# Performance work log

Measured on AMD Instinct MI355X. Metric: run time of the kernel, lower is better.

## Reference

```python
import jax, jax.numpy as jnp
import numpy as np

N_NODES = 20000
N_EDGES = 320000
IN_F = 256
OUT_F = 64
HEADS = 4
ALPHA = 0.1  # leaky_relu negative slope


def setup_inputs() -> dict:
    key = jax.random.key(0)
    ks = jax.random.split(key, 8)
    return {
        "input1": jax.random.normal(ks[0], (N_NODES, IN_F), jnp.float32),
        "input2": jax.random.normal(ks[1], (N_NODES, IN_F), jnp.float32),
        # per-head params: Ws maps source feats -> target_out, Wt maps target feats -> source_out
        "Ws": jax.random.normal(ks[2], (HEADS, IN_F, OUT_F), jnp.float32) * 0.06,
        "Wt": jax.random.normal(ks[3], (HEADS, IN_F, OUT_F), jnp.float32) * 0.06,
        "a1": jax.random.normal(ks[4], (HEADS, 2 * OUT_F), jnp.float32) * 0.1,
        "a2": jax.random.normal(ks[5], (HEADS, 2 * OUT_F), jnp.float32) * 0.1,
        # COO nonzeros of A_opt [n_target, n_source]
        "tgt_idx": jax.random.randint(ks[6], (N_EDGES,), 0, N_NODES),
        "src_idx": jax.random.randint(ks[7], (N_EDGES,), 0, N_NODES),
    }


def _segment_softmax(scores, seg, num_segments):
    m = jax.lax.stop_gradient(jax.ops.segment_max(scores, seg, num_segments=num_segments))
    w = jnp.exp(scores - m[seg])
    d = jax.ops.segment_sum(w, seg, num_segments=num_segments)
    d = jnp.where(d == 0, 1.0, d)
    return w / d[seg]


def _head(x1, x2, Ws, Wt, a1, a2, src, tgt, n_s, n_t):
    s = x1 @ Ws  # [n_s, OUT_F]  messages source -> target
    t = x2 @ Wt  # [n_t, OUT_F]  messages target -> source
    out = Ws.shape[1]
    # edge score e = leaky_relu(a^T [s_src || t_tgt]); split a to avoid edge-level concat
    e1 = jax.nn.leaky_relu((s @ a1[:out])[src] + (t @ a1[out:])[tgt], ALPHA)
    e2 = jax.nn.leaky_relu((s @ a2[:out])[src] + (t @ a2[out:])[tgt], ALPHA)
    alpha_ts = _segment_softmax(e1, tgt, n_t)  # softmax over sources per target
    alpha_st = _segment_softmax(e2, src, n_s)  # softmax over targets per source
    h_ts = jax.ops.segment_sum(alpha_ts[:, None] * s[src], tgt, num_segments=n_t)
    h_st = jax.ops.segment_sum(alpha_st[:, None] * t[tgt], src, num_segments=n_s)
    return jax.nn.elu(h_st), jax.nn.elu(h_ts)  # concat=True -> ELU per head


def reference(input1, input2, Ws, Wt, a1, a2, tgt_idx, src_idx):
    n_s, n_t = input1.shape[0], input2.shape[0]
    head_fn = jax.vmap(
        lambda W1, W2, v1, v2: _head(input1, input2, W1, W2, v1, v2, src_idx, tgt_idx, n_s, n_t)
    )
    h_st, h_ts = head_fn(Ws, Wt, a1, a2)  # each [H, n, OUT_F]
    h_st = jnp.transpose(h_st, (1, 0, 2)).reshape(n_s, -1)  # concat heads
    h_ts = jnp.transpose(h_ts, (1, 0, 2)).reshape(n_t, -1)
    return h_st, h_ts
```

## Files before the change

kernel.cpp:

```cpp
#include <hip/hip_runtime.h>
#include <math.h>

#define N_NODES 20000
#define N_EDGES 320000
#define IN_F 256
#define OUT_F 64
#define HEADS 4
#define NCOL 256
#define LRELU_ALPHA 0.1f
#define ELL_CAP 64

#define SCAT_X 313
#define GEMM_GB 157
#define CST_STRIDE 136

typedef __attribute__((ext_vector_type(8))) short short8;
typedef __attribute__((ext_vector_type(4))) float floatx4;

__device__ __forceinline__ float lrelu(float x) {
    return x > 0.f ? x : LRELU_ALPHA * x;
}
__device__ __forceinline__ unsigned short f2bf(float f) {
    unsigned int u = __float_as_uint(f);
    u = (u + 0x7FFF + ((u >> 16) & 1)) >> 16;
    return (unsigned short)u;
}
__device__ __forceinline__ float bf2f(unsigned short u) {
    return __uint_as_float(((unsigned int)u) << 16);
}

__global__ __launch_bounds__(256) void prep_w_kernel(
    const float* __restrict__ Ws, const float* __restrict__ Wt,
    unsigned short* __restrict__ Wsb, unsigned short* __restrict__ Wtb,
    int* __restrict__ cnt)
{
    const int gid = blockIdx.x * 256 + threadIdx.x;

    for (int i = gid; i < 2 * N_NODES; i += 16384) cnt[i] = 0;

    const int mat = gid >> 13;
    const int r   = gid & 8191;
    const int kc  = r >> 8;
    const int c   = r & 255;
    const float* W    = mat ? Wt : Ws;
    unsigned short* O = mat ? Wtb : Wsb;
    const int h = c >> 6, j = c & 63;
    const int k0 = kc * 8;
    unsigned short v[8] __attribute__((aligned(16)));
#pragma unroll
    for (int i = 0; i < 8; ++i)
        v[i] = f2bf(W[(size_t)h * (IN_F * OUT_F) + (size_t)(k0 + i) * OUT_F + j]);
    *(uint4*)(O + (size_t)c * IN_F + k0) = *(const uint4*)v;
}

__global__ __launch_bounds__(512, 4) void hybrid_kernel(
    const float* __restrict__ A0, const unsigned short* __restrict__ Wb0,
    const float* __restrict__ A1, const unsigned short* __restrict__ Wb1,
    unsigned short* __restrict__ C0, unsigned short* __restrict__ C1,
    const float* __restrict__ a1, const float* __restrict__ a2,
    float* __restrict__ ss1, float* __restrict__ ss2,
    float* __restrict__ tt1, float* __restrict__ tt2,
    const int* __restrict__ src, const int* __restrict__ tgt,
    int* __restrict__ cnt_t, int* __restrict__ cnt_s,
    unsigned short* __restrict__ elist_t, unsigned short* __restrict__ elist_s)
{
    const int tid = threadIdx.x;

    __shared__ __align__(16) unsigned short Bl[128][264];

    if (blockIdx.x < SCAT_X) {
        const int e = ((int)blockIdx.y * SCAT_X + (int)blockIdx.x) * 512 + tid;
        if (e < N_EDGES) {
            const int s = src[e], t = tgt[e];
            const int p = atomicAdd(&cnt_t[t], 1);
            const int q = atomicAdd(&cnt_s[s], 1);
            if (p < ELL_CAP) elist_t[t * ELL_CAP + p] = (unsigned short)s;
            if (q < ELL_CAP) elist_s[s * ELL_CAP + q] = (unsigned short)t;
        }
        return;
    }

    const int gx   = blockIdx.x - SCAT_X;
    const int half = gx & 1;
    const int gb   = gx >> 1;
    const float* A           = (blockIdx.y == 0) ? A0 : A1;
    const unsigned short* Wb = (blockIdx.y == 0) ? Wb0 : Wb1;
    unsigned short* C        = (blockIdx.y == 0) ? C0 : C1;

    for (int i = tid; i < 4096; i += 512) {
        const int n  = i >> 5;
        const int kc = (i & 31) << 3;
        *(uint4*)&Bl[n][kc] = *(const uint4*)(Wb + (size_t)(half * 128 + n) * IN_F + kc);
    }
    __syncthreads();

    const int lane = tid & 63;
    const int w    = tid >> 6;
    const int quad = lane >> 4;
    const int l15  = lane & 15;
    const int g    = gb * 8 + w;
    const bool live = (g < 1250);

    floatx4 acc[8];
#pragma unroll
    for (int c = 0; c < 8; ++c) acc[c] = (floatx4){0.f, 0.f, 0.f, 0.f};

    if (live) {
        const float* arow = A + (size_t)(g * 16 + l15) * IN_F + quad * 8;

        float4 ua[8];
#pragma unroll
        for (int kk = 0; kk < 4; ++kk) {
            ua[2 * kk]     = *(const float4*)(arow + kk * 32);
            ua[2 * kk + 1] = *(const float4*)(arow + kk * 32 + 4);
        }
        short8 af[4];
#pragma unroll
        for (int kk = 0; kk < 4; ++kk) {
            short8 t;
            t[0] = (short)f2bf(ua[2 * kk].x);     t[1] = (short)f2bf(ua[2 * kk].y);
            t[2] = (short)f2bf(ua[2 * kk].z);     t[3] = (short)f2bf(ua[2 * kk].w);
            t[4] = (short)f2bf(ua[2 * kk + 1].x); t[5] = (short)f2bf(ua[2 * kk + 1].y);
            t[6] = (short)f2bf(ua[2 * kk + 1].z); t[7] = (short)f2bf(ua[2 * kk + 1].w);
            af[kk] = t;
        }

        float4 ub[8];
#pragma unroll
        for (int kk = 0; kk < 4; ++kk) {
            ub[2 * kk]     = *(const float4*)(arow + (kk + 4) * 32);
            ub[2 * kk + 1] = *(const float4*)(arow + (kk + 4) * 32 + 4);
        }

#pragma unroll
        for (int kk = 0; kk < 4; ++kk) {
#pragma unroll
            for (int c = 0; c < 8; ++c) {
                short8 bfrag = *(const short8*)&Bl[c * 16 + l15][kk * 32 + quad * 8];
                acc[c] = __builtin_amdgcn_mfma_f32_16x16x32_bf16(af[kk], bfrag, acc[c], 0, 0, 0);
            }
        }

#pragma unroll
        for (int kk = 0; kk < 4; ++kk) {
            short8 t;
            t[0] = (short)f2bf(ub[2 * kk].x);     t[1] = (short)f2bf(ub[2 * kk].y);
            t[2] = (short)f2bf(ub[2 * kk].z);     t[3] = (short)f2bf(ub[2 * kk].w);
            t[4] = (short)f2bf(ub[2 * kk + 1].x); t[5] = (short)f2bf(ub[2 * kk + 1].y);
            t[6] = (short)f2bf(ub[2 * kk + 1].z); t[7] = (short)f2bf(ub[2 * kk + 1].w);
            af[kk] = t;
        }
#pragma unroll
        for (int kk = 0; kk < 4; ++kk) {
#pragma unroll
            for (int c = 0; c < 8; ++c) {
                short8 bfrag = *(const short8*)&Bl[c * 16 + l15][(kk + 4) * 32 + quad * 8];
                acc[c] = __builtin_amdgcn_mfma_f32_16x16x32_bf16(af[kk], bfrag, acc[c], 0, 0, 0);
            }
        }

        const int off_aj = (blockIdx.y == 0) ? 0 : 64;
        float* o1 = (blockIdx.y == 0) ? ss1 : tt1;
        float* o2 = (blockIdx.y == 0) ? ss2 : tt2;

        float p1[2][4] = {{0.f,0.f,0.f,0.f},{0.f,0.f,0.f,0.f}};
        float p2[2][4] = {{0.f,0.f,0.f,0.f},{0.f,0.f,0.f,0.f}};
#pragma unroll
        for (int c = 0; c < 8; ++c) {
            const int hl = c >> 2;
            const int hh = half * 2 + hl;
            const int jj = (c & 3) * 16 + l15;
            const float w1 = a1[hh * 128 + off_aj + jj];
            const float w2 = a2[hh * 128 + off_aj + jj];
#pragma unroll
            for (int r = 0; r < 4; ++r) {
                p1[hl][r] += acc[c][r] * w1;
                p2[hl][r] += acc[c][r] * w2;
            }
        }
#pragma unroll
        for (int m = 1; m < 16; m <<= 1) {
#pragma unroll
            for (int hl = 0; hl < 2; ++hl)
#pragma unroll
                for (int r = 0; r < 4; ++r) {
                    p1[hl][r] += __shfl_xor(p1[hl][r], m, 64);
                    p2[hl][r] += __shfl_xor(p2[hl][r], m, 64);
                }
        }
        if (l15 == 0) {
#pragma unroll
            for (int r = 0; r < 4; ++r) {
                const int m = g * 16 + quad * 4 + r;
#pragma unroll
                for (int hl = 0; hl < 2; ++hl) {
                    const int hh = half * 2 + hl;
                    o1[m * HEADS + hh] = p1[hl][r];
                    o2[m * HEADS + hh] = p2[hl][r];
                }
            }
        }
    }

    __syncthreads();
    unsigned short* Cst = &Bl[0][0];

    if (live) {
#pragma unroll
        for (int c = 0; c < 8; ++c) {
            const int lc = c * 16 + l15;
#pragma unroll
            for (int r = 0; r < 4; ++r) {
                const int lr = w * 16 + quad * 4 + r;
                Cst[lr * CST_STRIDE + lc] = f2bf(acc[c][r]);
            }
        }
    }
    __syncthreads();

    {
        const int cx = tid & 15;
        const int rbase = tid >> 4;
#pragma unroll
        for (int it = 0; it < 4; ++it) {
            const int lr = it * 32 + rbase;
            const int mrow = gb * 128 + lr;
            if (mrow < N_NODES) {
                uint4 v = *(const uint4*)&Cst[lr * CST_STRIDE + cx * 8];
                *(uint4*)(C + (size_t)mrow * NCOL + half * 128 + cx * 8) = v;
            }
        }
    }
}

__global__ __launch_bounds__(256) void agg_kernel(
    const int* __restrict__ cnt_t, const unsigned short* __restrict__ elist_t,
    const int* __restrict__ cnt_s, const unsigned short* __restrict__ elist_s,
    const float* __restrict__ ss1, const float* __restrict__ ss2,
    const float* __restrict__ tt1, const float* __restrict__ tt2,
    const unsigned short* __restrict__ s_bf, const unsigned short* __restrict__ t_bf,
    float* __restrict__ h_st, float* __restrict__ h_ts)
{
    const int b    = blockIdx.x;
    const int dir  = b & 1;
    const int wave = threadIdx.x >> 6;
    const int lane = threadIdx.x & 63;
    const int n    = (b >> 1) * 4 + wave;
    const int h    = lane >> 4;
    const int coff = lane * 4;

    const int*            cnt   = dir ? cnt_s   : cnt_t;
    const unsigned short* list  = dir ? elist_s : elist_t;
    const unsigned short* table = dir ? t_bf    : s_bf;
    const float*          nsc   = dir ? ss2     : tt1;
    const float*          esc   = dir ? tt2     : ss1;
    float*                outp  = dir ? h_st    : h_ts;

    __shared__ __align__(16) uint2 wm[4][64][4];

    int deg = cnt[n];
    if (deg > ELL_CAP) deg = ELL_CAP;
    const unsigned short* lp = list + n * ELL_CAP;

    {
        const int  mraw = lp[lane];
        const bool act  = lane < deg;
        const int  m    = act ? mraw : 0;
        const float4 e4 = *(const float4*)(esc + m * HEADS);
        const float4 b4 = *(const float4*)(nsc + n * HEADS);
        const float w0 = act ? __expf(lrelu(e4.x + b4.x)) : 0.f;
        const float w1 = act ? __expf(lrelu(e4.y + b4.y)) : 0.f;
        const float w2 = act ? __expf(lrelu(e4.z + b4.z)) : 0.f;
        const float w3 = act ? __expf(lrelu(e4.w + b4.w)) : 0.f;
        const unsigned off = (unsigned)(m * (NCOL * 2));
        wm[wave][lane][0] = make_uint2(__float_as_uint(w0), off);
        wm[wave][lane][1] = make_uint2(__float_as_uint(w1), off);
        wm[wave][lane][2] = make_uint2(__float_as_uint(w2), off);
        wm[wave][lane][3] = make_uint2(__float_as_uint(w3), off);
    }

    __syncthreads();

    const uint2* wrow = &wm[wave][0][h];
    const char*  tb   = (const char*)table;
    const unsigned cb = (unsigned)(coff * 2);

    float4 acc = make_float4(0.f, 0.f, 0.f, 0.f);
    float den = 0.f;

    int p = 0;
    for (; p + 3 < deg; p += 4) {
        uint2 a0 = wrow[(p + 0) * 4];
        uint2 a1 = wrow[(p + 1) * 4];
        uint2 a2 = wrow[(p + 2) * 4];
        uint2 a3 = wrow[(p + 3) * 4];
        float w0 = __uint_as_float(a0.x);
        float w1 = __uint_as_float(a1.x);
        float w2 = __uint_as_float(a2.x);
        float w3 = __uint_as_float(a3.x);
        ushort4 r0 = *(const ushort4*)(tb + (a0.y + cb));
        ushort4 r1 = *(const ushort4*)(tb + (a1.y + cb));
        ushort4 r2 = *(const ushort4*)(tb + (a2.y + cb));
        ushort4 r3 = *(const ushort4*)(tb + (a3.y + cb));
        den += (w0 + w1) + (w2 + w3);
        acc.x += (w0 * bf2f(r0.x) + w1 * bf2f(r1.x)) + (w2 * bf2f(r2.x) + w3 * bf2f(r3.x));
        acc.y += (w0 * bf2f(r0.y) + w1 * bf2f(r1.y)) + (w2 * bf2f(r2.y) + w3 * bf2f(r3.y));
        acc.z += (w0 * bf2f(r0.z) + w1 * bf2f(r1.z)) + (w2 * bf2f(r2.z) + w3 * bf2f(r3.z));
        acc.w += (w0 * bf2f(r0.w) + w1 * bf2f(r1.w)) + (w2 * bf2f(r2.w) + w3 * bf2f(r3.w));
    }
    for (; p < deg; ++p) {
        uint2 a0 = wrow[p * 4];
        float w0 = __uint_as_float(a0.x);
        ushort4 r0 = *(const ushort4*)(tb + (a0.y + cb));
        den += w0;
        acc.x += w0 * bf2f(r0.x);
        acc.y += w0 * bf2f(r0.y);
        acc.z += w0 * bf2f(r0.z);
        acc.w += w0 * bf2f(r0.w);
    }

    if (den == 0.f) den = 1.f;
    float inv = 1.f / den;
    float4 r;
    r.x = acc.x * inv; r.y = acc.y * inv; r.z = acc.z * inv; r.w = acc.w * inv;
    r.x = (r.x > 0.f) ? r.x : expm1f(r.x);
    r.y = (r.y > 0.f) ? r.y : expm1f(r.y);
    r.z = (r.z > 0.f) ? r.z : expm1f(r.z);
    r.w = (r.w > 0.f) ? r.w : expm1f(r.w);
    *(float4*)(outp + (size_t)n * NCOL + coff) = r;
}

extern "C" void kernel_launch(void* const* d_in, const int* in_sizes, int n_in,
                              void* d_out, int out_size, void* d_ws, size_t ws_size,
                              hipStream_t stream)
{
    const float* input1 = (const float*)d_in[0];
    const float* input2 = (const float*)d_in[1];
    const float* Ws     = (const float*)d_in[2];
    const float* Wt     = (const float*)d_in[3];
    const float* a1     = (const float*)d_in[4];
    const float* a2     = (const float*)d_in[5];
    const int*   tgt    = (const int*)d_in[6];
    const int*   src    = (const int*)d_in[7];

    float* out  = (float*)d_out;
    float* h_st = out;
    float* h_ts = out + (size_t)N_NODES * NCOL;

    unsigned short* s_bf = (unsigned short*)d_ws;
    unsigned short* t_bf = s_bf + (size_t)N_NODES * NCOL;
    unsigned short* Wsb  = t_bf + (size_t)N_NODES * NCOL;
    unsigned short* Wtb  = Wsb + 256 * 256;
    float* ss1  = (float*)(Wtb + 256 * 256);
    float* ss2  = ss1 + N_NODES * HEADS;
    float* tt1  = ss2 + N_NODES * HEADS;
    float* tt2  = tt1 + N_NODES * HEADS;
    int*   cnt_t = (int*)(tt2 + N_NODES * HEADS);
    int*   cnt_s = cnt_t + N_NODES;
    unsigned short* elist_t = (unsigned short*)(cnt_s + N_NODES);
    unsigned short* elist_s = elist_t + (size_t)N_NODES * ELL_CAP;

    prep_w_kernel<<<64, 256, 0, stream>>>(Ws, Wt, Wsb, Wtb, cnt_t);

    dim3 ggrid(SCAT_X + GEMM_GB * 2, 2);
    hybrid_kernel<<<ggrid, 512, 0, stream>>>(input1, Wsb, input2, Wtb,
                                             s_bf, t_bf, a1, a2,
                                             ss1, ss2, tt1, tt2,
                                             src, tgt, cnt_t, cnt_s,
                                             elist_t, elist_s);

    agg_kernel<<<10000, 256, 0, stream>>>(cnt_t, elist_t, cnt_s, elist_s,
                                          ss1, ss2, tt1, tt2, s_bf, t_bf,
                                          h_st, h_ts);
}
```

Measured before the change: 178.0 us.

## Split GEMM column tiles into quarters and unroll aggregation gather by eight

The fused GEMM now gives each block a 64-column quarter (one head) of the weights instead of a 128-column half. That halves shared memory and accumulator registers per block and doubles the number of GEMM blocks, aiming for higher occupancy and parallelism. The cost is that each block rereads its A rows four times instead of twice. The aggregation loop also gains an 8-way unrolled path so more gather loads are in flight at once, at the price of more registers.

```diff
diff --git a/kernel.cpp b/kernel.cpp
--- a/kernel.cpp
+++ b/kernel.cpp
@@ -11,8 +11,8 @@
 #define ELL_CAP 64
 
 #define SCAT_X 313
-#define GEMM_GB 157
-#define CST_STRIDE 136
+#define GEMM_QX 628
+#define CSTQ 72
 
 typedef __attribute__((ext_vector_type(8))) short short8;
 typedef __attribute__((ext_vector_type(4))) float floatx4;
@@ -66,7 +66,7 @@
 {
     const int tid = threadIdx.x;
 
-    __shared__ __align__(16) unsigned short Bl[128][264];
+    __shared__ __align__(16) unsigned short Bl[64][264];
 
     if (blockIdx.x < SCAT_X) {
         const int e = ((int)blockIdx.y * SCAT_X + (int)blockIdx.x) * 512 + tid;
@@ -81,16 +81,16 @@
     }
 
     const int gx   = blockIdx.x - SCAT_X;
-    const int half = gx & 1;
-    const int gb   = gx >> 1;
+    const int qtr  = gx & 3;
+    const int gb   = gx >> 2;
     const float* A           = (blockIdx.y == 0) ? A0 : A1;
     const unsigned short* Wb = (blockIdx.y == 0) ? Wb0 : Wb1;
     unsigned short* C        = (blockIdx.y == 0) ? C0 : C1;
 
-    for (int i = tid; i < 4096; i += 512) {
+    for (int i = tid; i < 2048; i += 512) {
         const int n  = i >> 5;
         const int kc = (i & 31) << 3;
-        *(uint4*)&Bl[n][kc] = *(const uint4*)(Wb + (size_t)(half * 128 + n) * IN_F + kc);
+        *(uint4*)&Bl[n][kc] = *(const uint4*)(Wb + (size_t)(qtr * 64 + n) * IN_F + kc);
     }
     __syncthreads();
 
@@ -101,9 +101,9 @@
     const int g    = gb * 8 + w;
     const bool live = (g < 1250);
 
-    floatx4 acc[8];
-#pragma unroll
-    for (int c = 0; c < 8; ++c) acc[c] = (floatx4){0.f, 0.f, 0.f, 0.f};
+    floatx4 acc[4];
+#pragma unroll
+    for (int c = 0; c < 4; ++c) acc[c] = (floatx4){0.f, 0.f, 0.f, 0.f};
 
     if (live) {
         const float* arow = A + (size_t)(g * 16 + l15) * IN_F + quad * 8;
@@ -135,7 +135,7 @@
 #pragma unroll
         for (int kk = 0; kk < 4; ++kk) {
 #pragma unroll
-            for (int c = 0; c < 8; ++c) {
+            for (int c = 0; c < 4; ++c) {
                 short8 bfrag = *(const short8*)&Bl[c * 16 + l15][kk * 32 + quad * 8];
                 acc[c] = __builtin_amdgcn_mfma_f32_16x16x32_bf16(af[kk], bfrag, acc[c], 0, 0, 0);
             }
@@ -153,7 +153,7 @@
 #pragma unroll
         for (int kk = 0; kk < 4; ++kk) {
 #pragma unroll
-            for (int c = 0; c < 8; ++c) {
+            for (int c = 0; c < 4; ++c) {
                 short8 bfrag = *(const short8*)&Bl[c * 16 + l15][(kk + 4) * 32 + quad * 8];
                 acc[c] = __builtin_amdgcn_mfma_f32_16x16x32_bf16(af[kk], bfrag, acc[c], 0, 0, 0);
             }
@@ -163,41 +163,33 @@
         float* o1 = (blockIdx.y == 0) ? ss1 : tt1;
         float* o2 = (blockIdx.y == 0) ? ss2 : tt2;
 
-        float p1[2][4] = {{0.f,0.f,0.f,0.f},{0.f,0.f,0.f,0.f}};
-        float p2[2][4] = {{0.f,0.f,0.f,0.f},{0.f,0.f,0.f,0.f}};
-#pragma unroll
-        for (int c = 0; c < 8; ++c) {
-            const int hl = c >> 2;
-            const int hh = half * 2 + hl;
-            const int jj = (c & 3) * 16 + l15;
-            const float w1 = a1[hh * 128 + off_aj + jj];
-            const float w2 = a2[hh * 128 + off_aj + jj];
+        float p1[4] = {0.f, 0.f, 0.f, 0.f};
+        float p2[4] = {0.f, 0.f, 0.f, 0.f};
+#pragma unroll
+        for (int c = 0; c < 4; ++c) {
+            const int jj = c * 16 + l15;
+            const float w1 = a1[qtr * 128 + off_aj + jj];
+            const float w2 = a2[qtr * 128 + off_aj + jj];
 #pragma unroll
             for (int r = 0; r < 4; ++r) {
-                p1[hl][r] += acc[c][r] * w1;
-                p2[hl][r] += acc[c][r] * w2;
+                p1[r] += acc[c][r] * w1;
+                p2[r] += acc[c][r] * w2;
             }
         }
 #pragma unroll
         for (int m = 1; m < 16; m <<= 1) {
 #pragma unroll
-            for (int hl = 0; hl < 2; ++hl)
-#pragma unroll
-                for (int r = 0; r < 4; ++r) {
-                    p1[hl][r] += __shfl_xor(p1[hl][r], m, 64);
-                    p2[hl][r] += __shfl_xor(p2[hl][r], m, 64);
-                }
+            for (int r = 0; r < 4; ++r) {
+                p1[r] += __shfl_xor(p1[r], m, 64);
+                p2[r] += __shfl_xor(p2[r], m, 64);
+            }
         }
         if (l15 == 0) {
 #pragma unroll
             for (int r = 0; r < 4; ++r) {
                 const int m = g * 16 + quad * 4 + r;
-#pragma unroll
-                for (int hl = 0; hl < 2; ++hl) {
-                    const int hh = half * 2 + hl;
-                    o1[m * HEADS + hh] = p1[hl][r];
-                    o2[m * HEADS + hh] = p2[hl][r];
-                }
+                o1[m * HEADS + qtr] = p1[r];
+                o2[m * HEADS + qtr] = p2[r];
             }
         }
     }
@@ -207,27 +199,27 @@
 
     if (live) {
 #pragma unroll
-        for (int c = 0; c < 8; ++c) {
+        for (int c = 0; c < 4; ++c) {
             const int lc = c * 16 + l15;
 #pragma unroll
             for (int r = 0; r < 4; ++r) {
                 const int lr = w * 16 + quad * 4 + r;
-                Cst[lr * CST_STRIDE + lc] = f2bf(acc[c][r]);
+                Cst[lr * CSTQ + lc] = f2bf(acc[c][r]);
             }
         }
     }
     __syncthreads();
 
     {
-        const int cx = tid & 15;
-        const int rbase = tid >> 4;
-#pragma unroll
-        for (int it = 0; it < 4; ++it) {
-            const int lr = it * 32 + rbase;
+#pragma unroll
+        for (int it = 0; it < 2; ++it) {
+            const int id  = it * 512 + tid;
+            const int lr  = id >> 3;
+            const int cq  = id & 7;
             const int mrow = gb * 128 + lr;
             if (mrow < N_NODES) {
-                uint4 v = *(const uint4*)&Cst[lr * CST_STRIDE + cx * 8];
-                *(uint4*)(C + (size_t)mrow * NCOL + half * 128 + cx * 8) = v;
+                uint4 v = *(const uint4*)&Cst[lr * CSTQ + cq * 8];
+                *(uint4*)(C + (size_t)mrow * NCOL + qtr * 64 + cq * 8) = v;
             }
         }
     }
@@ -289,15 +281,44 @@
     float den = 0.f;
 
     int p = 0;
+    for (; p + 7 < deg; p += 8) {
+        uint2 a0 = wrow[(p + 0) * 4];
+        uint2 a1 = wrow[(p + 1) * 4];
+        uint2 a2 = wrow[(p + 2) * 4];
+        uint2 a3 = wrow[(p + 3) * 4];
+        uint2 a4 = wrow[(p + 4) * 4];
+        uint2 a5 = wrow[(p + 5) * 4];
+        uint2 a6 = wrow[(p + 6) * 4];
+        uint2 a7 = wrow[(p + 7) * 4];
+        float w0 = __uint_as_float(a0.x), w1 = __uint_as_float(a1.x);
+        float w2 = __uint_as_float(a2.x), w3 = __uint_as_float(a3.x);
+        float w4 = __uint_as_float(a4.x), w5 = __uint_as_float(a5.x);
+        float w6 = __uint_as_float(a6.x), w7 = __uint_as_float(a7.x);
+        ushort4 r0 = *(const ushort4*)(tb + (a0.y + cb));
+        ushort4 r1 = *(const ushort4*)(tb + (a1.y + cb));
+        ushort4 r2 = *(const ushort4*)(tb + (a2.y + cb));
+        ushort4 r3 = *(const ushort4*)(tb + (a3.y + cb));
+        ushort4 r4 = *(const ushort4*)(tb + (a4.y + cb));
+        ushort4 r5 = *(const ushort4*)(tb + (a5.y + cb));
+        ushort4 r6 = *(const ushort4*)(tb + (a6.y + cb));
+        ushort4 r7 = *(const ushort4*)(tb + (a7.y + cb));
+        den += ((w0 + w1) + (w2 + w3)) + ((w4 + w5) + (w6 + w7));
+        acc.x += ((w0 * bf2f(r0.x) + w1 * bf2f(r1.x)) + (w2 * bf2f(r2.x) + w3 * bf2f(r3.x)))
+               + ((w4 * bf2f(r4.x) + w5 * bf2f(r5.x)) + (w6 * bf2f(r6.x) + w7 * bf2f(r7.x)));
+        acc.y += ((w0 * bf2f(r0.y) + w1 * bf2f(r1.y)) + (w2 * bf2f(r2.y) + w3 * bf2f(r3.y)))
+               + ((w4 * bf2f(r4.y) + w5 * bf2f(r5.y)) + (w6 * bf2f(r6.y) + w7 * bf2f(r7.y)));
+        acc.z += ((w0 * bf2f(r0.z) + w1 * bf2f(r1.z)) + (w2 * bf2f(r2.z) + w3 * bf2f(r3.z)))
+               + ((w4 * bf2f(r4.z) + w5 * bf2f(r5.z)) + (w6 * bf2f(r6.z) + w7 * bf2f(r7.z)));
+        acc.w += ((w0 * bf2f(r0.w) + w1 * bf2f(r1.w)) + (w2 * bf2f(r2.w) + w3 * bf2f(r3.w)))
+               + ((w4 * bf2f(r4.w) + w5 * bf2f(r5.w)) + (w6 * bf2f(r6.w) + w7 * bf2f(r7.w)));
+    }
     for (; p + 3 < deg; p += 4) {
         uint2 a0 = wrow[(p + 0) * 4];
         uint2 a1 = wrow[(p + 1) * 4];
         uint2 a2 = wrow[(p + 2) * 4];
         uint2 a3 = wrow[(p + 3) * 4];
-        float w0 = __uint_as_float(a0.x);
-        float w1 = __uint_as_float(a1.x);
-        float w2 = __uint_as_float(a2.x);
-        float w3 = __uint_as_float(a3.x);
+        float w0 = __uint_as_float(a0.x), w1 = __uint_as_float(a1.x);
+        float w2 = __uint_as_float(a2.x), w3 = __uint_as_float(a3.x);
         ushort4 r0 = *(const ushort4*)(tb + (a0.y + cb));
         ushort4 r1 = *(const ushort4*)(tb + (a1.y + cb));
         ushort4 r2 = *(const ushort4*)(tb + (a2.y + cb));
@@ -362,7 +383,7 @@
 
     prep_w_kernel<<<64, 256, 0, stream>>>(Ws, Wt, Wsb, Wtb, cnt_t);
 
-    dim3 ggrid(SCAT_X + GEMM_GB * 2, 2);
+    dim3 ggrid(SCAT_X + GEMM_QX, 2);
     hybrid_kernel<<<ggrid, 512, 0, stream>>>(input1, Wsb, input2, Wtb,
                                              s_bf, t_bf, a1, a2,
                                              ss1, ss2, tt1, tt2,
```

New measurement: 187.6 us. 1.05x slower.

## Fuse weight bf16 conversion into GEMM tile load and unroll aggregation by eight

Applied to the files above, without the earlier changes.

Removes the separate prep kernel: each GEMM block now reads fp32 Ws/Wt directly, converts to bf16 and transposes into shared memory, and the counter zeroing becomes a hipMemsetAsync. This drops one kernel launch and the intermediate bf16 weight buffer round trip, at the cost of redundant conversion work in every GEMM block. The aggregation inner loop also gains an 8-way unrolled path to expose more independent gathers per iteration, which may raise register pressure.

```diff
diff --git a/kernel.cpp b/kernel.cpp
--- a/kernel.cpp
+++ b/kernel.cpp
@@ -29,33 +29,9 @@
     return __uint_as_float(((unsigned int)u) << 16);
 }
 
-__global__ __launch_bounds__(256) void prep_w_kernel(
-    const float* __restrict__ Ws, const float* __restrict__ Wt,
-    unsigned short* __restrict__ Wsb, unsigned short* __restrict__ Wtb,
-    int* __restrict__ cnt)
-{
-    const int gid = blockIdx.x * 256 + threadIdx.x;
-
-    for (int i = gid; i < 2 * N_NODES; i += 16384) cnt[i] = 0;
-
-    const int mat = gid >> 13;
-    const int r   = gid & 8191;
-    const int kc  = r >> 8;
-    const int c   = r & 255;
-    const float* W    = mat ? Wt : Ws;
-    unsigned short* O = mat ? Wtb : Wsb;
-    const int h = c >> 6, j = c & 63;
-    const int k0 = kc * 8;
-    unsigned short v[8] __attribute__((aligned(16)));
-#pragma unroll
-    for (int i = 0; i < 8; ++i)
-        v[i] = f2bf(W[(size_t)h * (IN_F * OUT_F) + (size_t)(k0 + i) * OUT_F + j]);
-    *(uint4*)(O + (size_t)c * IN_F + k0) = *(const uint4*)v;
-}
-
 __global__ __launch_bounds__(512, 4) void hybrid_kernel(
-    const float* __restrict__ A0, const unsigned short* __restrict__ Wb0,
-    const float* __restrict__ A1, const unsigned short* __restrict__ Wb1,
+    const float* __restrict__ A0, const float* __restrict__ W0,
+    const float* __restrict__ A1, const float* __restrict__ W1,
     unsigned short* __restrict__ C0, unsigned short* __restrict__ C1,
     const float* __restrict__ a1, const float* __restrict__ a2,
     float* __restrict__ ss1, float* __restrict__ ss2,
@@ -83,14 +59,31 @@
     const int gx   = blockIdx.x - SCAT_X;
     const int half = gx & 1;
     const int gb   = gx >> 1;
-    const float* A           = (blockIdx.y == 0) ? A0 : A1;
-    const unsigned short* Wb = (blockIdx.y == 0) ? Wb0 : Wb1;
-    unsigned short* C        = (blockIdx.y == 0) ? C0 : C1;
-
-    for (int i = tid; i < 4096; i += 512) {
-        const int n  = i >> 5;
-        const int kc = (i & 31) << 3;
-        *(uint4*)&Bl[n][kc] = *(const uint4*)(Wb + (size_t)(half * 128 + n) * IN_F + kc);
+    const float* A    = (blockIdx.y == 0) ? A0 : A1;
+    const float* Wsrc = (blockIdx.y == 0) ? W0 : W1;
+    unsigned short* C = (blockIdx.y == 0) ? C0 : C1;
+
+    for (int it = 0; it < 4; ++it) {
+        const int cid = it * 512 + tid;
+        const int hh  = cid >> 10;
+        const int rem = cid & 1023;
+        const int kg  = rem >> 4;
+        const int j4  = (rem & 15) << 2;
+        const float* base = Wsrc + (size_t)(half * 2 + hh) * (IN_F * OUT_F)
+                          + (size_t)(kg * 4) * OUT_F + j4;
+        float a0[4], a1v[4], a2v[4], a3[4];
+        *(float4*)a0  = *(const float4*)(base);
+        *(float4*)a1v = *(const float4*)(base + OUT_F);
+        *(float4*)a2v = *(const float4*)(base + 2 * OUT_F);
+        *(float4*)a3  = *(const float4*)(base + 3 * OUT_F);
+#pragma unroll
+        for (int i = 0; i < 4; ++i) {
+            const int n0 = hh * 64 + j4 + i;
+            unsigned short q[4] __attribute__((aligned(8)));
+            q[0] = f2bf(a0[i]); q[1] = f2bf(a1v[i]);
+            q[2] = f2bf(a2v[i]); q[3] = f2bf(a3[i]);
+            *(uint2*)&Bl[n0][kg * 4] = *(const uint2*)q;
+        }
     }
     __syncthreads();
 
@@ -289,15 +282,44 @@
     float den = 0.f;
 
     int p = 0;
+    for (; p + 7 < deg; p += 8) {
+        uint2 a0 = wrow[(p + 0) * 4];
+        uint2 a1 = wrow[(p + 1) * 4];
+        uint2 a2 = wrow[(p + 2) * 4];
+        uint2 a3 = wrow[(p + 3) * 4];
+        uint2 a4 = wrow[(p + 4) * 4];
+        uint2 a5 = wrow[(p + 5) * 4];
+        uint2 a6 = wrow[(p + 6) * 4];
+        uint2 a7 = wrow[(p + 7) * 4];
+        float w0 = __uint_as_float(a0.x), w1 = __uint_as_float(a1.x);
+        float w2 = __uint_as_float(a2.x), w3 = __uint_as_float(a3.x);
+        float w4 = __uint_as_float(a4.x), w5 = __uint_as_float(a5.x);
+        float w6 = __uint_as_float(a6.x), w7 = __uint_as_float(a7.x);
+        ushort4 r0 = *(const ushort4*)(tb + (a0.y + cb));
+        ushort4 r1 = *(const ushort4*)(tb + (a1.y + cb));
+        ushort4 r2 = *(const ushort4*)(tb + (a2.y + cb));
+        ushort4 r3 = *(const ushort4*)(tb + (a3.y + cb));
+        ushort4 r4 = *(const ushort4*)(tb + (a4.y + cb));
+        ushort4 r5 = *(const ushort4*)(tb + (a5.y + cb));
+        ushort4 r6 = *(const ushort4*)(tb + (a6.y + cb));
+        ushort4 r7 = *(const ushort4*)(tb + (a7.y + cb));
+        den += ((w0 + w1) + (w2 + w3)) + ((w4 + w5) + (w6 + w7));
+        acc.x += ((w0 * bf2f(r0.x) + w1 * bf2f(r1.x)) + (w2 * bf2f(r2.x) + w3 * bf2f(r3.x)))
+               + ((w4 * bf2f(r4.x) + w5 * bf2f(r5.x)) + (w6 * bf2f(r6.x) + w7 * bf2f(r7.x)));
+        acc.y += ((w0 * bf2f(r0.y) + w1 * bf2f(r1.y)) + (w2 * bf2f(r2.y) + w3 * bf2f(r3.y)))
+               + ((w4 * bf2f(r4.y) + w5 * bf2f(r5.y)) + (w6 * bf2f(r6.y) + w7 * bf2f(r7.y)));
+        acc.z += ((w0 * bf2f(r0.z) + w1 * bf2f(r1.z)) + (w2 * bf2f(r2.z) + w3 * bf2f(r3.z)))
+               + ((w4 * bf2f(r4.z) + w5 * bf2f(r5.z)) + (w6 * bf2f(r6.z) + w7 * bf2f(r7.z)));
+        acc.w += ((w0 * bf2f(r0.w) + w1 * bf2f(r1.w)) + (w2 * bf2f(r2.w) + w3 * bf2f(r3.w)))
+               + ((w4 * bf2f(r4.w) + w5 * bf2f(r5.w)) + (w6 * bf2f(r6.w) + w7 * bf2f(r7.w)));
+    }
     for (; p + 3 < deg; p += 4) {
         uint2 a0 = wrow[(p + 0) * 4];
         uint2 a1 = wrow[(p + 1) * 4];
         uint2 a2 = wrow[(p + 2) * 4];
         uint2 a3 = wrow[(p + 3) * 4];
-        float w0 = __uint_as_float(a0.x);
-        float w1 = __uint_as_float(a1.x);
-        float w2 = __uint_as_float(a2.x);
-        float w3 = __uint_as_float(a3.x);
+        float w0 = __uint_as_float(a0.x), w1 = __uint_as_float(a1.x);
+        float w2 = __uint_as_float(a2.x), w3 = __uint_as_float(a3.x);
         ushort4 r0 = *(const ushort4*)(tb + (a0.y + cb));
         ushort4 r1 = *(const ushort4*)(tb + (a1.y + cb));
         ushort4 r2 = *(const ushort4*)(tb + (a2.y + cb));
@@ -360,10 +382,10 @@
     unsigned short* elist_t = (unsigned short*)(cnt_s + N_NODES);
     unsigned short* elist_s = elist_t + (size_t)N_NODES * ELL_CAP;
 
-    prep_w_kernel<<<64, 256, 0, stream>>>(Ws, Wt, Wsb, Wtb, cnt_t);
+    hipMemsetAsync(cnt_t, 0, 2 * N_NODES * sizeof(int), stream);
 
     dim3 ggrid(SCAT_X + GEMM_GB * 2, 2);
-    hybrid_kernel<<<ggrid, 512, 0, stream>>>(input1, Wsb, input2, Wtb,
+    hybrid_kernel<<<ggrid, 512, 0, stream>>>(input1, Ws, input2, Wt,
                                              s_bf, t_bf, a1, a2,
                                              ss1, ss2, tt1, tt2,
                                              src, tgt, cnt_t, cnt_s,
```

New measurement: 179.6 us. Within noise of the previous version (+0.9%).
